# Kernel tuning notes

Measured on AMD Instinct MI355X. Metric: run time of the kernel, lower is better.

The kernel has to match this reference:

```python
import jax, jax.numpy as jnp
import numpy as np

D_MODEL = 1024
HEAD_DIM = 64

def setup_inputs() -> dict:
    key = jax.random.key(0)
    ks = jax.random.split(key, 7)
    x = jax.random.normal(ks[0], (4, 4096, D_MODEL), dtype=jnp.float32)
    s = 1.0 / np.sqrt(D_MODEL)
    Wq = jax.random.uniform(ks[1], (D_MODEL, HEAD_DIM), jnp.float32, -s, s)
    bq = jax.random.uniform(ks[2], (HEAD_DIM,), jnp.float32, -s, s)
    Wk = jax.random.uniform(ks[3], (D_MODEL, HEAD_DIM), jnp.float32, -s, s)
    bk = jax.random.uniform(ks[4], (HEAD_DIM,), jnp.float32, -s, s)
    Wv = jax.random.uniform(ks[5], (D_MODEL, HEAD_DIM), jnp.float32, -s, s)
    bv = jax.random.uniform(ks[6], (HEAD_DIM,), jnp.float32, -s, s)
    return {"x": x, "Wq": Wq, "bq": bq, "Wk": Wk, "bk": bk, "Wv": Wv, "bv": bv}

def reference(x, Wq, bq, Wk, bk, Wv, bv):
    B, T, _ = x.shape
    q = x @ Wq + bq  # [B, T, H]
    k = x @ Wk + bk
    v = x @ Wv + bv
    scale = 1.0 / jnp.sqrt(jnp.asarray(q.shape[-1], q.dtype))
    scores = jnp.einsum('bqh,bkh->bqk', q, k) * scale  # [B, T, T]
    causal = jnp.tril(jnp.ones((T, T), dtype=bool))
    scores = jnp.where(causal, scores, jnp.asarray(-jnp.inf, scores.dtype))
    attn = jax.nn.softmax(scores, axis=-1)
    return jnp.einsum('bqk,bkh->bqh', attn, v)
```

## Files before the change

### kernel.cpp

```cpp
#include <hip/hip_runtime.h>

#define BATCH 4
#define SEQ 4096
#define DMODEL 1024
#define HDIM 64

#define QBLK 64
#define NQT 64
#define CHUNK 256
#define ITERS 8
#define BSLOT 544
#define MAXC 17

#define QSCALE 0.18033688f

typedef _Float16 h16;
typedef _Float16 h16x8 __attribute__((ext_vector_type(8)));
typedef _Float16 h16x4 __attribute__((ext_vector_type(4)));
typedef float f32x4 __attribute__((ext_vector_type(4)));
typedef float f32x16 __attribute__((ext_vector_type(16)));

#define WF_ELEMS (12 * 32 * 64 * 8)
#define QK_ELEMS (BATCH * SEQ * HDIM)
#define PB 262144
#define NSLOT (BATCH * BSLOT)

__device__ __forceinline__ int slot_base(int qt) {
    int a = qt >> 2, b = qt & 3;
    return (a + 1) * (2 * a + b);
}

__device__ __forceinline__ int kperm(int u) {
    return (u & 3) | (((u >> 2) & 1) << 3) | (((u >> 3) & 1) << 2);
}

template<int OFF>
__device__ __forceinline__ void gload_o(h16x8& dst, const h16* p) {
    asm volatile("global_load_dwordx4 %0, %1, off offset:%2" : "=v"(dst) : "v"(p), "n"(OFF));
}
template<int OFF>
__device__ __forceinline__ void gloadf_o(f32x4& dst, const float* p) {
    asm volatile("global_load_dwordx4 %0, %1, off offset:%2" : "=v"(dst) : "v"(p), "n"(OFF));
}

#define MFMA16(a, b, c) __builtin_amdgcn_mfma_f32_16x16x32_f16(a, b, c, 0, 0, 0)

__global__ __launch_bounds__(256) void prep_w(const float* __restrict__ Wq,
                                              const float* __restrict__ Wk,
                                              const float* __restrict__ Wv,
                                              h16* __restrict__ Wf) {
    int flat = blockIdx.x * 256 + threadIdx.x;
    int lane = flat & 63;
    int kt = (flat >> 6) & 31;
    int fg = flat >> 11;
    int col = 16 * fg + (lane & 15);
    const float* W = (col < 64) ? Wq : (col < 128) ? Wk : Wv;
    int c = col & 63;
    int k0 = 32 * kt + 8 * (lane >> 4);
    h16x8 v;
    #pragma unroll
    for (int j = 0; j < 8; j++) v[j] = (h16)W[(size_t)(k0 + j) * 64 + c];
    *(h16x8*)(Wf + (size_t)flat * 8) = v;
}

#define XISSUE(R, S) { gloadf_o<(S) * 256>(R##a, xp); gloadf_o<(S) * 256 + 16>(R##b, xp); }

#define WISSUE(S) {                                                           \
    gload_o<0>(wr##S##0, w0); gload_o<1024>(wr##S##1, w0);                    \
    gload_o<0>(wr##S##2, w1); gload_o<1024>(wr##S##3, w1);                    \
    gload_o<0>(wr##S##4, w2); gload_o<1024>(wr##S##5, w2);                    \
    w0 += 1024; w1 += 1024; w2 += 1024; }

#define XWRITE(R, P) {                                                        \
    h16x8 v_;                                                                 \
    _Pragma("unroll")                                                         \
    for (int j_ = 0; j_ < 4; j_++) { v_[j_] = (h16)R##a[j_]; v_[4 + j_] = (h16)R##b[j_]; } \
    *(h16x8*)(&xbuf[P][wo]) = v_; }

#define QCOMP(S, P) {                                                         \
    h16x8 a00 = *(const h16x8*)(&xbuf[P][lane * 8]);                          \
    h16x8 a01 = *(const h16x8*)(&xbuf[P][512 + lane * 8]);                    \
    c00 = MFMA16(a00, wr##S##0, c00); c01 = MFMA16(a00, wr##S##2, c01);       \
    c02 = MFMA16(a00, wr##S##4, c02);                                         \
    c10 = MFMA16(a01, wr##S##0, c10); c11 = MFMA16(a01, wr##S##2, c11);       \
    c12 = MFMA16(a01, wr##S##4, c12);                                         \
    h16x8 a10 = *(const h16x8*)(&xbuf[P][1024 + lane * 8]);                   \
    h16x8 a11 = *(const h16x8*)(&xbuf[P][1536 + lane * 8]);                   \
    c00 = MFMA16(a10, wr##S##1, c00); c01 = MFMA16(a10, wr##S##3, c01);       \
    c02 = MFMA16(a10, wr##S##5, c02);                                         \
    c10 = MFMA16(a11, wr##S##1, c10); c11 = MFMA16(a11, wr##S##3, c11);       \
    c12 = MFMA16(a11, wr##S##5, c12); }

#define VM0 { asm volatile("s_waitcnt vmcnt(0)" ::: "memory");                \
              __builtin_amdgcn_sched_barrier(0); }

#define STGE(s) { QCOMP(A, 0) VM0 XWRITE(xB, 1) XISSUE(xA, (s) + 2) WISSUE(A) __syncthreads(); }
#define STGO(s) { QCOMP(B, 1) VM0 XWRITE(xA, 0) XISSUE(xB, (s) + 2) WISSUE(B) __syncthreads(); }

__global__ __launch_bounds__(256, 2) void qkv_fused(
    const float* __restrict__ x, const h16* __restrict__ Wf,
    const float* __restrict__ bq, const float* __restrict__ bk, const float* __restrict__ bv,
    h16* __restrict__ Qf, h16* __restrict__ Kf, h16* __restrict__ Vf)
{
    __shared__ h16 xbuf[2][2048];
    int t = threadIdx.x;
    int lane = t & 63;
    int w = t >> 6;
    int r0 = blockIdx.x * 32;
    int ln15 = lane & 15;

    const float* xp = x + (size_t)(r0 + (t >> 3)) * DMODEL + (t & 7) * 8;
    int wo = ((t & 7) >> 2) * 1024 + ((t >> 3) >> 4) * 512 +
             ((t & 3) * 16 + ((t >> 3) & 15)) * 8;
    const h16* w0 = Wf + (size_t)(3 * w) * 16384 + lane * 8;
    const h16* w1 = w0 + 16384;
    const h16* w2 = w0 + 32768;

    f32x4 xAa, xAb, xBa, xBb;
    h16x8 wrA0, wrA1, wrA2, wrA3, wrA4, wrA5;
    h16x8 wrB0, wrB1, wrB2, wrB3, wrB4, wrB5;
    f32x4 c00 = {}, c01 = {}, c02 = {}, c10 = {}, c11 = {}, c12 = {};

    XISSUE(xA, 0) WISSUE(A) XISSUE(xB, 1) WISSUE(B)
    asm volatile("s_waitcnt vmcnt(8)" ::: "memory");
    __builtin_amdgcn_sched_barrier(0);
    XWRITE(xA, 0)
    __syncthreads();

    STGE(0)  STGO(1)  STGE(2)  STGO(3)
    STGE(4)  STGO(5)  STGE(6)  STGO(7)
    STGE(8)  STGO(9)  STGE(10) STGO(11)
    STGE(12) STGO(13)
    { QCOMP(A, 0) VM0 XWRITE(xB, 1) __syncthreads(); }
    { QCOMP(B, 1) }

    f32x4 acc[2][3] = {{c00, c01, c02}, {c10, c11, c12}};
    #pragma unroll
    for (int f = 0; f < 3; f++) {
        int col = 48 * w + 16 * f + ln15;
        float bias = (col < 64) ? bq[col] : (col < 128) ? bk[col - 64] : bv[col - 128];
        #pragma unroll
        for (int m = 0; m < 2; m++) {
            #pragma unroll
            for (int i = 0; i < 4; i++) {
                int tr = r0 + 16 * m + (lane >> 4) * 4 + i;
                int bb = tr >> 12;
                int tt = tr & (SEQ - 1);
                float v = acc[m][f][i] + bias;
                if (col < 64) {
                    int d = col >> 4, hh = (col >> 3) & 1, e = col & 7;
                    Qf[(size_t)bb * PB + (tt >> 5) * 2048 + d * 512 +
                       (hh * 32 + (tt & 31)) * 8 + e] = (h16)(v * QSCALE);
                } else if (col < 128) {
                    int ck = col - 64;
                    int d = ck >> 4, hh = (ck >> 3) & 1, e = ck & 7;
                    Kf[(size_t)bb * PB + (tt >> 5) * 2048 + d * 512 +
                       (hh * 32 + (tt & 31)) * 8 + e] = (h16)v;
                } else {
                    int h = col - 128;
                    int tp = (tt & ~15) | kperm(tt & 15);
                    int j = ((h >> 5) << 1) | ((tp >> 4) & 1);
                    Vf[(size_t)bb * PB + (tp >> 5) * 2048 + j * 512 +
                       (((tp >> 3) & 1) * 32 + (h & 31)) * 8 + (tp & 7)] = (h16)v;
                }
            }
        }
    }
}

__device__ __forceinline__ void flash_compute(
    h16x8 K0, h16x8 K1, h16x8 K2, h16x8 K3,
    h16x8 V0, h16x8 V1, h16x8 V2, h16x8 V3,
    h16x8 q0v, h16x8 q1v, h16x8 q2v, h16x8 q3v,
    int kt0, int q0g, int qg, int hi,
    f32x16& o0, f32x16& o1, float& m_i, float& l_i)
{
    f32x16 s = {};
    s = __builtin_amdgcn_mfma_f32_32x32x16_f16(K0, q0v, s, 0, 0, 0);
    s = __builtin_amdgcn_mfma_f32_32x32x16_f16(K1, q1v, s, 0, 0, 0);
    s = __builtin_amdgcn_mfma_f32_32x32x16_f16(K2, q2v, s, 0, 0, 0);
    s = __builtin_amdgcn_mfma_f32_32x32x16_f16(K3, q3v, s, 0, 0, 0);

    float sc[16];
    #pragma unroll
    for (int r = 0; r < 16; r++) sc[r] = s[r];
    if (kt0 + 31 > q0g) {
        #pragma unroll
        for (int r = 0; r < 16; r++) {
            int kg = kt0 + (r & 3) + 8 * (r >> 2) + 4 * hi;
            if (kg > qg) sc[r] = -1e30f;
        }
    }
    float tm = sc[0];
    #pragma unroll
    for (int r = 1; r < 16; r++) tm = fmaxf(tm, sc[r]);
    tm = fmaxf(tm, __shfl_xor(tm, 32));

    if (!__all(tm - m_i <= 8.f)) {
        float mn = fmaxf(m_i, tm);
        float al = exp2f(m_i - mn);
        m_i = mn;
        l_i *= al;
        #pragma unroll
        for (int r = 0; r < 16; r++) { o0[r] *= al; o1[r] *= al; }
    }

    float p[16], rs = 0.f;
    #pragma unroll
    for (int r = 0; r < 16; r++) { p[r] = exp2f(sc[r] - m_i); rs += p[r]; }
    rs += __shfl_xor(rs, 32);
    l_i += rs;

    h16x8 pb0, pb1;
    #pragma unroll
    for (int j = 0; j < 8; j++) { pb0[j] = (h16)p[j]; pb1[j] = (h16)p[8 + j]; }

    o0 = __builtin_amdgcn_mfma_f32_32x32x16_f16(V0, pb0, o0, 0, 0, 0);
    o0 = __builtin_amdgcn_mfma_f32_32x32x16_f16(V1, pb1, o0, 0, 0, 0);
    o1 = __builtin_amdgcn_mfma_f32_32x32x16_f16(V2, pb0, o1, 0, 0, 0);
    o1 = __builtin_amdgcn_mfma_f32_32x32x16_f16(V3, pb1, o1, 0, 0, 0);
}

#define ISSUE(B) {                                                            \
    gload_o<0>(k##B##0, kp);    gload_o<1024>(k##B##1, kp);                   \
    gload_o<2048>(k##B##2, kp); gload_o<3072>(k##B##3, kp);                   \
    gload_o<0>(v##B##0, vp);    gload_o<1024>(v##B##1, vp);                   \
    gload_o<2048>(v##B##2, vp); gload_o<3072>(v##B##3, vp);                   \
    kp += 2048; vp += 2048; }

#define COMPUTE(B, T) {                                                       \
    __builtin_amdgcn_s_setprio(1);                                            \
    flash_compute(k##B##0, k##B##1, k##B##2, k##B##3,                         \
                  v##B##0, v##B##1, v##B##2, v##B##3,                         \
                  qa0, qa1, qa2, qa3, S + 32 * (T), q0, qg0, hi,              \
                  o00, o01, m0, l0);                                          \
    flash_compute(k##B##0, k##B##1, k##B##2, k##B##3,                         \
                  v##B##0, v##B##1, v##B##2, v##B##3,                         \
                  qc0, qc1, qc2, qc3, S + 32 * (T), q0 + 32, qg1, hi,         \
                  o10, o11, m1, l1);                                          \
    __builtin_amdgcn_s_setprio(0); }

#define STEP(CUR, NXT, T) {                                                   \
    ISSUE(NXT)                                                                \
    asm volatile("s_waitcnt vmcnt(8)" ::: "memory");                          \
    __builtin_amdgcn_sched_barrier(0);                                        \
    COMPUTE(CUR, T) }

#define STEP_LAST(CUR, T) {                                                   \
    asm volatile("s_waitcnt vmcnt(0)" ::: "memory");                          \
    __builtin_amdgcn_sched_barrier(0);                                        \
    COMPUTE(CUR, T) }

__global__ __launch_bounds__(256, 2) void flash(
    const h16* __restrict__ Qf, const h16* __restrict__ Kf, const h16* __restrict__ Vf,
    h16* __restrict__ o_part, float* __restrict__ ml_part)
{
    int wid = threadIdx.x >> 6;
    int lane = threadIdx.x & 63;
    int bid = blockIdx.x;
    int batch = bid / 136;
    int s = bid - batch * 136;
    int a = (int)((sqrtf(8.f * s + 1.f) - 1.f) * 0.5f);
    while ((a + 1) * (a + 2) / 2 <= s) a++;
    while (a * (a + 1) / 2 > s) a--;
    int c = s - a * (a + 1) / 2;
    int qt = 4 * a + wid;

    int q0 = qt * QBLK;
    int S = c * CHUNK;
    int l31 = lane & 31;
    int hi = lane >> 5;
    int qg0 = q0 + l31;
    int qg1 = q0 + 32 + l31;

    const h16* kp = Kf + (size_t)batch * PB + (S >> 5) * 2048 + lane * 8;
    const h16* vp = Vf + (size_t)batch * PB + (S >> 5) * 2048 + lane * 8;

    h16x8 qa0, qa1, qa2, qa3, qc0, qc1, qc2, qc3;
    {
        const h16* qp = Qf + (size_t)batch * PB + (q0 >> 5) * 2048 + lane * 8;
        gload_o<0>(qa0, qp); gload_o<1024>(qa1, qp);
        gload_o<2048>(qa2, qp); gload_o<3072>(qa3, qp);
        const h16* qp2 = qp + 2048;
        gload_o<0>(qc0, qp2); gload_o<1024>(qc1, qp2);
        gload_o<2048>(qc2, qp2); gload_o<3072>(qc3, qp2);
    }

    h16x8 kA0, kA1, kA2, kA3, vA0, vA1, vA2, vA3;
    h16x8 kB0, kB1, kB2, kB3, vB0, vB1, vB2, vB3;

    f32x16 o00 = {}, o01 = {}, o10 = {}, o11 = {};
    float m0 = -1e30f, l0 = 0.f, m1 = -1e30f, l1 = 0.f;

    ISSUE(A)

    STEP(A, B, 0)
    STEP(B, A, 1)
    STEP(A, B, 2)
    STEP(B, A, 3)
    STEP(A, B, 4)
    STEP(B, A, 5)
    STEP(A, B, 6)
    STEP_LAST(B, 7)

    size_t slot = (size_t)batch * BSLOT + slot_base(qt) + c;
    h16* opb = o_part + slot * (QBLK * 64);
    {
        float inv = 1.f / l0;
        h16* op = opb + l31 * 64;
        #pragma unroll
        for (int q = 0; q < 4; q++) {
            h16x4 pk0, pk1;
            #pragma unroll
            for (int i = 0; i < 4; i++) {
                pk0[i] = (h16)(o00[4 * q + i] * inv);
                pk1[i] = (h16)(o01[4 * q + i] * inv);
            }
            *(h16x4*)(op + 8 * q + 4 * hi) = pk0;
            *(h16x4*)(op + 32 + 8 * q + 4 * hi) = pk1;
        }
    }
    {
        float inv = 1.f / l1;
        h16* op = opb + (32 + l31) * 64;
        #pragma unroll
        for (int q = 0; q < 4; q++) {
            h16x4 pk0, pk1;
            #pragma unroll
            for (int i = 0; i < 4; i++) {
                pk0[i] = (h16)(o10[4 * q + i] * inv);
                pk1[i] = (h16)(o11[4 * q + i] * inv);
            }
            *(h16x4*)(op + 8 * q + 4 * hi) = pk0;
            *(h16x4*)(op + 32 + 8 * q + 4 * hi) = pk1;
        }
    }
    if (hi == 0) {
        ml_part[slot * 128 + l31 * 2] = m0;
        ml_part[slot * 128 + l31 * 2 + 1] = l0;
        ml_part[slot * 128 + (32 + l31) * 2] = m1;
        ml_part[slot * 128 + (32 + l31) * 2 + 1] = l1;
    }
}

__global__ __launch_bounds__(256) void combine(
    const h16* __restrict__ o_part, const float* __restrict__ ml_part,
    float* __restrict__ out)
{
    __shared__ float mlds[MAXC * 128];
    int bid = blockIdx.x;
    int rq = bid & 3;
    int tile = bid >> 2;
    int batch = tile >> 6;
    int qt = tile & (NQT - 1);
    int q0 = qt * QBLK;
    int nc = (qt >> 2) + 1;
    size_t base = (size_t)batch * BSLOT + slot_base(qt);

    for (int i = threadIdx.x; i < nc * 128; i += 256)
        mlds[i] = ml_part[base * 128 + i];
    __syncthreads();

    int r = rq * 16 + (threadIdx.x >> 4);
    int c4 = (threadIdx.x & 15) * 4;

    float M = -1e30f;
    for (int c = 0; c < nc; c++) M = fmaxf(M, mlds[c * 128 + r * 2]);

    const h16* op = o_part + base * (QBLK * 64) + r * 64 + c4;
    float L = 0.f;
    f32x4 A = {};
    #pragma unroll 4
    for (int c = 0; c < nc; c++) {
        float wt = exp2f(mlds[c * 128 + r * 2] - M) * mlds[c * 128 + r * 2 + 1];
        L += wt;
        h16x4 v = *(const h16x4*)(op + (size_t)c * (QBLK * 64));
        A[0] += wt * (float)v[0];
        A[1] += wt * (float)v[1];
        A[2] += wt * (float)v[2];
        A[3] += wt * (float)v[3];
    }
    f32x4 o;
    float inv = 1.f / L;
    #pragma unroll
    for (int j = 0; j < 4; j++) o[j] = A[j] * inv;
    *(f32x4*)(out + ((size_t)batch * SEQ + q0 + r) * HDIM + c4) = o;
}

extern "C" void kernel_launch(void* const* d_in, const int* in_sizes, int n_in,
                              void* d_out, int out_size, void* d_ws, size_t ws_size,
                              hipStream_t stream) {
    const float* x  = (const float*)d_in[0];
    const float* Wq = (const float*)d_in[1];
    const float* bq = (const float*)d_in[2];
    const float* Wk = (const float*)d_in[3];
    const float* bk = (const float*)d_in[4];
    const float* Wv = (const float*)d_in[5];
    const float* bv = (const float*)d_in[6];
    float* out = (float*)d_out;

    h16* Wf = (h16*)d_ws;
    h16* Qf = Wf + WF_ELEMS;
    h16* Kf = Qf + QK_ELEMS;
    h16* Vf = Kf + QK_ELEMS;
    h16* o_part = Vf + QK_ELEMS;
    float* ml_part = (float*)(o_part + (size_t)NSLOT * QBLK * 64);

    hipLaunchKernelGGL(prep_w, dim3(96), dim3(256), 0, stream, Wq, Wk, Wv, Wf);
    hipLaunchKernelGGL(qkv_fused, dim3(512), dim3(256), 0, stream,
                       x, Wf, bq, bk, bv, Qf, Kf, Vf);
    hipLaunchKernelGGL(flash, dim3(BATCH * 136), dim3(256), 0, stream,
                       Qf, Kf, Vf, o_part, ml_part);
    hipLaunchKernelGGL(combine, dim3(BATCH * NQT * 4), dim3(256), 0, stream,
                       o_part, ml_part, out);
}
```

Before: 62.32 us.

## Fuse split-K combine into flash kernel via atomic last-arriver counter

```diff
diff --git a/kernel.cpp b/kernel.cpp
--- a/kernel.cpp
+++ b/kernel.cpp
@@ -10,7 +10,6 @@
 #define CHUNK 256
 #define ITERS 8
 #define BSLOT 544
-#define MAXC 17
 
 #define QSCALE 0.18033688f
 
@@ -48,7 +47,9 @@
 __global__ __launch_bounds__(256) void prep_w(const float* __restrict__ Wq,
                                               const float* __restrict__ Wk,
                                               const float* __restrict__ Wv,
-                                              h16* __restrict__ Wf) {
+                                              h16* __restrict__ Wf,
+                                              int* __restrict__ cnt) {
+    if (blockIdx.x == 0) cnt[threadIdx.x] = 0;
     int flat = blockIdx.x * 256 + threadIdx.x;
     int lane = flat & 63;
     int kt = (flat >> 6) & 31;
@@ -253,7 +254,8 @@
 
 __global__ __launch_bounds__(256, 2) void flash(
     const h16* __restrict__ Qf, const h16* __restrict__ Kf, const h16* __restrict__ Vf,
-    h16* __restrict__ o_part, float* __restrict__ ml_part)
+    h16* __restrict__ o_part, float* __restrict__ ml_part,
+    int* __restrict__ cnt, float* __restrict__ out)
 {
     int wid = threadIdx.x >> 6;
     int lane = threadIdx.x & 63;
@@ -341,50 +343,45 @@
         ml_part[slot * 128 + (32 + l31) * 2] = m1;
         ml_part[slot * 128 + (32 + l31) * 2 + 1] = l1;
     }
-}
-
-__global__ __launch_bounds__(256) void combine(
-    const h16* __restrict__ o_part, const float* __restrict__ ml_part,
-    float* __restrict__ out)
-{
-    __shared__ float mlds[MAXC * 128];
-    int bid = blockIdx.x;
-    int rq = bid & 3;
-    int tile = bid >> 2;
-    int batch = tile >> 6;
-    int qt = tile & (NQT - 1);
-    int q0 = qt * QBLK;
-    int nc = (qt >> 2) + 1;
-    size_t base = (size_t)batch * BSLOT + slot_base(qt);
-
-    for (int i = threadIdx.x; i < nc * 128; i += 256)
-        mlds[i] = ml_part[base * 128 + i];
-    __syncthreads();
-
-    int r = rq * 16 + (threadIdx.x >> 4);
-    int c4 = (threadIdx.x & 15) * 4;
-
+
+    __threadfence();
+    int old = 0;
+    if (lane == 0) old = atomicAdd(&cnt[batch * NQT + qt], 1);
+    old = __shfl(old, 0);
+    if (old != a) return;
+    __threadfence();
+
+    int r = lane;
+    size_t qbase = (size_t)batch * BSLOT + slot_base(qt);
     float M = -1e30f;
-    for (int c = 0; c < nc; c++) M = fmaxf(M, mlds[c * 128 + r * 2]);
-
-    const h16* op = o_part + base * (QBLK * 64) + r * 64 + c4;
+    for (int cc = 0; cc <= a; cc++)
+        M = fmaxf(M, ml_part[(qbase + cc) * 128 + r * 2]);
+
+    float A[64];
+    #pragma unroll
+    for (int j = 0; j < 64; j++) A[j] = 0.f;
     float L = 0.f;
-    f32x4 A = {};
-    #pragma unroll 4
-    for (int c = 0; c < nc; c++) {
-        float wt = exp2f(mlds[c * 128 + r * 2] - M) * mlds[c * 128 + r * 2 + 1];
+    for (int cc = 0; cc <= a; cc++) {
+        float wt = exp2f(ml_part[(qbase + cc) * 128 + r * 2] - M) *
+                   ml_part[(qbase + cc) * 128 + r * 2 + 1];
         L += wt;
-        h16x4 v = *(const h16x4*)(op + (size_t)c * (QBLK * 64));
-        A[0] += wt * (float)v[0];
-        A[1] += wt * (float)v[1];
-        A[2] += wt * (float)v[2];
-        A[3] += wt * (float)v[3];
-    }
-    f32x4 o;
+        const h16* oprow = o_part + (qbase + cc) * (QBLK * 64) + r * 64;
+        #pragma unroll
+        for (int sg = 0; sg < 8; sg++) {
+            h16x8 v = *(const h16x8*)(oprow + sg * 8);
+            #pragma unroll
+            for (int j = 0; j < 8; j++) A[sg * 8 + j] += wt * (float)v[j];
+        }
+    }
     float inv = 1.f / L;
-    #pragma unroll
-    for (int j = 0; j < 4; j++) o[j] = A[j] * inv;
-    *(f32x4*)(out + ((size_t)batch * SEQ + q0 + r) * HDIM + c4) = o;
+    float* orow = out + ((size_t)batch * SEQ + q0 + r) * HDIM;
+    #pragma unroll
+    for (int sg = 0; sg < 16; sg++) {
+        f32x4 o;
+        #pragma unroll
+        for (int j = 0; j < 4; j++) o[j] = A[sg * 4 + j] * inv;
+        *(f32x4*)(orow + sg * 4) = o;
+    }
 }
 
 extern "C" void kernel_launch(void* const* d_in, const int* in_sizes, int n_in,
@@ -405,12 +402,11 @@
     h16* Vf = Kf + QK_ELEMS;
     h16* o_part = Vf + QK_ELEMS;
     float* ml_part = (float*)(o_part + (size_t)NSLOT * QBLK * 64);
-
-    hipLaunchKernelGGL(prep_w, dim3(96), dim3(256), 0, stream, Wq, Wk, Wv, Wf);
+    int* cnt = (int*)(ml_part + (size_t)NSLOT * 128);
+
+    hipLaunchKernelGGL(prep_w, dim3(96), dim3(256), 0, stream, Wq, Wk, Wv, Wf, cnt);
     hipLaunchKernelGGL(qkv_fused, dim3(512), dim3(256), 0, stream,
                        x, Wf, bq, bk, bv, Qf, Kf, Vf);
     hipLaunchKernelGGL(flash, dim3(BATCH * 136), dim3(256), 0, stream,
-                       Qf, Kf, Vf, o_part, ml_part);
-    hipLaunchKernelGGL(combine, dim3(BATCH * NQT * 4), dim3(256), 0, stream,
-                       o_part, ml_part, out);
-}
+                       Qf, Kf, Vf, o_part, ml_part, cnt, out);
+}
```

Result: slower. 179.6 us (+188.2%).
